# Performance work log

Measured on AMD Instinct MI355X. Metric: run time of the kernel, lower is better.

Reference implementation:

```python
import jax, jax.numpy as jnp
import numpy as np

LORA_DIM = 16          # hard-coded in module
LORA_TOKEN_INDEX = 1   # lora_dim*layer_sequence + 1 with layer_sequence=0
B, S, D, H = 4, 2048, 1024, 4096  # num_hiddens = 4*num_input (forced by view())


def setup_inputs() -> dict:
    key = jax.random.key(0)
    ks = jax.random.split(key, 6)
    x = jax.random.normal(ks[0], (B, S, D), dtype=jnp.float32)
    W1 = jax.random.normal(ks[1], (H, D), dtype=jnp.float32) * 0.02
    b1 = jnp.zeros((H,), dtype=jnp.float32)
    W2 = jax.random.normal(ks[2], (D, H), dtype=jnp.float32) * 0.02
    b2 = jnp.zeros((D,), dtype=jnp.float32)
    scale = jnp.asarray(0.001, dtype=jnp.float32)  # nn.Parameter(torch.tensor(0.001))
    return {"x": x, "W1": W1, "b1": b1, "W2": W2, "b2": b2, "scale": scale}


def reference(x, W1, b1, W2, b2, scale):
    Bx, Sx, Dx = x.shape
    Hx = W1.shape[0]  # = 4*Dx
    # 16 lora tokens starting at LORA_TOKEN_INDEX
    lt = jax.lax.dynamic_slice_in_dim(x, LORA_TOKEN_INDEX, LORA_DIM, axis=1)
    even = lt[:, ::2, :]  # (B, 8, D)
    odd = lt[:, 1::2, :]  # (B, 8, D)
    # per-sample low-rank weight updates:
    # result_multiplication[b,k] = outer(even[b,k], odd[b,k]) (D,D)
    # matrix1 = first 4 blocks stacked -> (B, 4D, D); matrix2 = last 4 reshaped -> (B, D, 4D)
    m1 = (even[:, :4, :, None] * odd[:, :4, None, :]).reshape(Bx, Hx, Dx)
    m2 = (even[:, 4:, :, None] * odd[:, 4:, None, :]).reshape(Bx, Dx, Hx)
    # x @ (W1 + scale*m1)^T + b1, fused without repeating W1 per batch
    h = jnp.einsum('bsd,hd->bsh', x, W1) + scale * jnp.einsum('bsd,bhd->bsh', x, m1) + b1
    h = jax.nn.gelu(h, approximate=False)  # torch nn.GELU default = exact erf
    out = jnp.einsum('bsh,oh->bso', h, W2) + scale * jnp.einsum('bsh,boh->bso', h, m2) + b2
    return out
```

## Files before the change

kernel.cpp:

```cpp
#include <hip/hip_runtime.h>
#include <cstdint>
#include <cstddef>

#define MROWS 8192
#define DDIM  1024
#define HDIM  4096

typedef __bf16 bf16x8 __attribute__((ext_vector_type(8)));
typedef float  f32x4  __attribute__((ext_vector_type(4)));

typedef __attribute__((address_space(1))) void* as1_vp;
typedef __attribute__((address_space(3))) void* as3_vp;

__device__ __forceinline__ unsigned short f2bf(float f) {
  unsigned int u = __builtin_bit_cast(unsigned int, f);
  u += 0x7fffu + ((u >> 16) & 1u);
  return (unsigned short)(u >> 16);
}
__device__ __forceinline__ float bf2f(unsigned short h) {
  return __builtin_bit_cast(float, (unsigned int)h << 16);
}

__device__ __forceinline__ float fast_gelu(float x) {
  float x3 = x * x * x;
  float z = 0.7978845608028654f * x + 0.03567740814f * x3;
  float e = __builtin_amdgcn_exp2f(z * 2.8853900817779268f);
  float t = 1.0f - 2.0f * __builtin_amdgcn_rcpf(e + 1.0f);
  return 0.5f * x * (1.0f + t);
}

__device__ __forceinline__ void gld_lds16(const unsigned short* g, unsigned short* lds) {
  __builtin_amdgcn_global_load_lds((as1_vp)(uintptr_t)g, (as3_vp)lds, 16, 0, 0);
}

#define VMW(n) asm volatile("s_waitcnt vmcnt(" #n ")" ::: "memory")
#define LKW()  asm volatile("s_waitcnt lgkmcnt(0)" ::: "memory")
#define BAR()  asm volatile("s_barrier" ::: "memory")

__global__ __launch_bounds__(256) void pre_kernel(
    const float* __restrict__ x, const float* __restrict__ w1,
    const float* __restrict__ w2, unsigned short* __restrict__ xb,
    unsigned short* __restrict__ w1b, unsigned short* __restrict__ w2b,
    float* __restrict__ p1) {
  if (blockIdx.x < 8192) {
    int i = blockIdx.x * 256 + threadIdx.x;
    const float* src; unsigned short* dst; int off;
    if (i < 1048576) { src = w1; dst = w1b; off = i; }
    else             { src = w2; dst = w2b; off = i - 1048576; }
    float4 v = ((const float4*)src)[off];
    ushort4 o;
    o.x = f2bf(v.x); o.y = f2bf(v.y); o.z = f2bf(v.z); o.w = f2bf(v.w);
    ((ushort4*)dst)[off] = o;
    return;
  }
  const int bid = blockIdx.x - 8192;
  const int wave = threadIdx.x >> 6, lane = threadIdx.x & 63;
  const int m = bid * 4 + wave;
  const int b = m >> 11;
  const float4* xrow4 = (const float4*)(x + (size_t)m * DDIM);
  const float4* od4   = (const float4*)(x + ((size_t)b * 2048 + 2) * DDIM);
  ushort4* xbrow4 = (ushort4*)(xb + (size_t)m * DDIM);
  float a0 = 0.f, a1 = 0.f, a2 = 0.f, a3 = 0.f;
#pragma unroll
  for (int it = 0; it < 4; ++it) {
    int g = it * 64 + lane;
    float4 v = xrow4[g];
    ushort4 o; o.x = f2bf(v.x); o.y = f2bf(v.y); o.z = f2bf(v.z); o.w = f2bf(v.w);
    xbrow4[g] = o;
    float4 o0 = od4[g];
    float4 o1 = od4[512 + g];
    float4 o2 = od4[1024 + g];
    float4 o3 = od4[1536 + g];
    a0 += v.x * o0.x + v.y * o0.y + v.z * o0.z + v.w * o0.w;
    a1 += v.x * o1.x + v.y * o1.y + v.z * o1.z + v.w * o1.w;
    a2 += v.x * o2.x + v.y * o2.y + v.z * o2.z + v.w * o2.w;
    a3 += v.x * o3.x + v.y * o3.y + v.z * o3.z + v.w * o3.w;
  }
#pragma unroll
  for (int off = 32; off > 0; off >>= 1) {
    a0 += __shfl_down(a0, off);
    a1 += __shfl_down(a1, off);
    a2 += __shfl_down(a2, off);
    a3 += __shfl_down(a3, off);
  }
  if (lane == 0) {
    float4 r; r.x = a0; r.y = a1; r.z = a2; r.w = a3;
    ((float4*)p1)[m] = r;
  }
}

__global__ __launch_bounds__(512, 2) void gemm1_kernel(
    const unsigned short* __restrict__ xb, const unsigned short* __restrict__ w1b,
    const float* __restrict__ x, const float* __restrict__ b1,
    const float* __restrict__ p1, const float* __restrict__ scale_p,
    unsigned short* __restrict__ hact) {
  __shared__ __align__(16) unsigned short As[4 * 256 * 32];
  __shared__ __align__(16) unsigned short Bs[4 * 256 * 32];

  const int id = blockIdx.x;
  const int xcd = id & 7, w = id >> 3;
  const int m0 = (xcd * 4 + (w & 3)) * 256;
  const int n0 = (w >> 2) * 256;

  const int tid  = threadIdx.x;
  const int wave = tid >> 6, lane = tid & 63;
  const int quad = lane >> 4, l16 = lane & 15;
  const int wm2  = wave >> 2;
  const int wn2  = wave & 3;

  const unsigned short *gA0, *gA1, *gB0, *gB1;
  {
    int idx = tid;
    int r = idx >> 2, sl = idx & 3, c = (sl - (r >> 1)) & 3;
    gA0 = xb  + (size_t)(m0 + r) * DDIM + c * 8;
    gB0 = w1b + (size_t)(n0 + r) * DDIM + c * 8;
    idx = 512 + tid;
    r = idx >> 2; sl = idx & 3; c = (sl - (r >> 1)) & 3;
    gA1 = xb  + (size_t)(m0 + r) * DDIM + c * 8;
    gB1 = w1b + (size_t)(n0 + r) * DDIM + c * 8;
  }
  const int ldsOff0 = (wave * 64) * 8;
  const int ldsOff1 = (512 + wave * 64) * 8;

#define STAGE1(tt, sb) do {                                   \
    const int _k = (tt) * 32;                                 \
    unsigned short* _a = &As[(sb) * 8192];                    \
    unsigned short* _b = &Bs[(sb) * 8192];                    \
    gld_lds16(gA0 + _k, _a + ldsOff0);                        \
    gld_lds16(gA1 + _k, _a + ldsOff1);                        \
    gld_lds16(gB0 + _k, _b + ldsOff0);                        \
    gld_lds16(gB1 + _k, _b + ldsOff1);                        \
  } while (0)

  f32x4 acc[8][4];
  const f32x4 z = {0.f, 0.f, 0.f, 0.f};
#pragma unroll
  for (int i = 0; i < 8; ++i)
#pragma unroll
    for (int j = 0; j < 4; ++j) acc[i][j] = z;

  auto compute_tile = [&](const unsigned short* __restrict__ Ab,
                          const unsigned short* __restrict__ Bb) {
    bf16x8 a[8], b[4];
#pragma unroll
    for (int j = 0; j < 4; ++j) {
      const int rb = wn2 * 64 + j * 16 + l16;
      b[j] = *(const bf16x8*)(Bb + rb * 32 + ((quad + (rb >> 1)) & 3) * 8);
    }
#pragma unroll
    for (int i = 0; i < 8; ++i) {
      const int ra = wm2 * 128 + i * 16 + l16;
      a[i] = *(const bf16x8*)(Ab + ra * 32 + ((quad + (ra >> 1)) & 3) * 8);
    }
    __builtin_amdgcn_s_setprio(1);
#pragma unroll
    for (int i = 0; i < 8; ++i)
#pragma unroll
      for (int j = 0; j < 4; ++j)
        acc[i][j] = __builtin_amdgcn_mfma_f32_16x16x32_bf16(a[i], b[j], acc[i][j], 0, 0, 0);
    __builtin_amdgcn_s_setprio(0);
  };

#define TILE_FULL(tt, cb, sb) do {                            \
    STAGE1((tt) + 3, sb);                                     \
    VMW(12);                                                  \
    BAR();                                                    \
    compute_tile(&As[(cb) * 8192], &Bs[(cb) * 8192]);         \
    LKW();                                                    \
    BAR();                                                    \
  } while (0)

  STAGE1(0, 0);
  STAGE1(1, 1);
  STAGE1(2, 2);

#pragma unroll 1
  for (int t = 0; t < 28; t += 4) {
    TILE_FULL(t + 0, 0, 3);
    TILE_FULL(t + 1, 1, 0);
    TILE_FULL(t + 2, 2, 1);
    TILE_FULL(t + 3, 3, 2);
  }
  TILE_FULL(28, 0, 3);
  VMW(8);  BAR(); compute_tile(&As[1 * 8192], &Bs[1 * 8192]);
  VMW(4);  BAR(); compute_tile(&As[2 * 8192], &Bs[2 * 8192]);
  VMW(0);  BAR(); compute_tile(&As[3 * 8192], &Bs[3 * 8192]);

  const float sc = scale_p[0];
  const int bidx = m0 >> 11;
  const int i1 = (n0 + wn2 * 64) >> 10;
  const float* exrow = x + ((size_t)(bidx * 2048 + 1 + 2 * i1)) * DDIM;

  float exv[4], b1v[4]; int nn[4];
#pragma unroll
  for (int j = 0; j < 4; ++j) {
    nn[j]  = n0 + wn2 * 64 + j * 16 + l16;
    exv[j] = exrow[nn[j] & 1023];
    b1v[j] = b1[nn[j]];
  }
#pragma unroll
  for (int i = 0; i < 8; ++i) {
#pragma unroll
    for (int r = 0; r < 4; ++r) {
      const int m = m0 + wm2 * 128 + i * 16 + quad * 4 + r;
      const float pv = p1[(size_t)m * 4 + i1] * sc;
#pragma unroll
      for (int j = 0; j < 4; ++j) {
        float v = acc[i][j][r] + b1v[j] + pv * exv[j];
        hact[(size_t)m * HDIM + nn[j]] = f2bf(fast_gelu(v));
      }
    }
  }
#undef TILE_FULL
#undef STAGE1
}

__global__ __launch_bounds__(512, 2) void gemm2_kernel(
    const unsigned short* __restrict__ hact, const unsigned short* __restrict__ w2b,
    const float* __restrict__ x, const float* __restrict__ b2,
    const float* __restrict__ scale_p, float* __restrict__ out) {
  __shared__ __align__(16) unsigned short As[3 * 256 * 64];
  __shared__ __align__(16) unsigned short Bs[3 * 128 * 64];
  __shared__ __align__(16) unsigned short od_lds[1024];
  __shared__ __align__(16) float p2s[256 * 4];

  const int id = blockIdx.x;
  const int xcd = id & 7, w = id >> 3;
  const int m0 = (xcd * 4 + (w & 3)) * 256;
  const int n0 = (w >> 2) * 128;
  const int tid = threadIdx.x;
  const int wave = tid >> 6, lane = tid & 63, quad = lane >> 4, l16 = lane & 15;
  const int wmq = (wave >> 1) * 64;
  const int wnq = (wave & 1) * 64;
  const bool hi = (wave & 1);
  const int bidx = m0 >> 11;
  const int i2 = n0 >> 8;

  if (tid < 256) {
    const float4* src = (const float4*)(x + ((size_t)(bidx * 2048 + 10 + 2 * i2)) * DDIM);
    float4 v = src[tid];
    ushort4 o; o.x = f2bf(v.x); o.y = f2bf(v.y); o.z = f2bf(v.z); o.w = f2bf(v.w);
    ((ushort4*)od_lds)[tid] = o;
  }
  LKW();

  f32x4 acc[4][4];
  const f32x4 z = {0.f, 0.f, 0.f, 0.f};
#pragma unroll
  for (int i = 0; i < 4; ++i)
#pragma unroll
    for (int j = 0; j < 4; ++j) acc[i][j] = z;
  f32x4 pacc[2] = {z, z};
  const bf16x8 zer8 = __builtin_bit_cast(bf16x8, z);

  const unsigned short *gA[4], *gB[2];
#pragma unroll
  for (int s = 0; s < 4; ++s) {
    int idx = (wave * 4 + s) * 64 + lane;
    int r = idx >> 3, sl = idx & 7, c = (sl - r) & 7;
    gA[s] = hact + (size_t)(m0 + r) * HDIM + c * 8;
  }
#pragma unroll
  for (int s = 0; s < 2; ++s) {
    int idx = (wave * 2 + s) * 64 + lane;
    int r = idx >> 3, sl = idx & 7, c = (sl - r) & 7;
    gB[s] = w2b + (size_t)(n0 + r) * HDIM + c * 8;
  }

#define STAGE2(tt, sb) do {                                   \
    const int _k = (tt) * 64;                                 \
    unsigned short* _a = &As[(sb) * 16384];                   \
    unsigned short* _b = &Bs[(sb) * 8192];                    \
    gld_lds16(gA[0] + _k, _a + (wave * 4 + 0) * 512);         \
    gld_lds16(gA[1] + _k, _a + (wave * 4 + 1) * 512);         \
    gld_lds16(gA[2] + _k, _a + (wave * 4 + 2) * 512);         \
    gld_lds16(gA[3] + _k, _a + (wave * 4 + 3) * 512);         \
    gld_lds16(gB[0] + _k, _b + (wave * 2 + 0) * 512);         \
    gld_lds16(gB[1] + _k, _b + (wave * 2 + 1) * 512);         \
  } while (0)

  auto compute_tile = [&](const unsigned short* __restrict__ Ab,
                          const unsigned short* __restrict__ Bb, int odk) {
#pragma unroll
    for (int kk = 0; kk < 64; kk += 32) {
      bf16x8 a[4], b[4];
      const int cb = (kk >> 3) + quad;
#pragma unroll
      for (int j = 0; j < 4; ++j) {
        const int rb = wnq + j * 16 + l16;
        b[j] = *(const bf16x8*)(Bb + rb * 64 + ((cb + rb) & 7) * 8);
      }
#pragma unroll
      for (int i = 0; i < 4; ++i) {
        const int ra = wmq + i * 16 + l16;
        a[i] = *(const bf16x8*)(Ab + ra * 64 + ((cb + ra) & 7) * 8);
      }
      {
        bf16x8 odv = *(const bf16x8*)(od_lds + odk + kk + quad * 8);
        bf16x8 bod = (l16 == 0) ? odv : zer8;
        bf16x8 pa0 = hi ? a[2] : a[0];
        bf16x8 pa1 = hi ? a[3] : a[1];
        pacc[0] = __builtin_amdgcn_mfma_f32_16x16x32_bf16(pa0, bod, pacc[0], 0, 0, 0);
        pacc[1] = __builtin_amdgcn_mfma_f32_16x16x32_bf16(pa1, bod, pacc[1], 0, 0, 0);
      }
      __builtin_amdgcn_s_setprio(1);
#pragma unroll
      for (int i = 0; i < 4; ++i)
#pragma unroll
        for (int j = 0; j < 4; ++j)
          acc[i][j] = __builtin_amdgcn_mfma_f32_16x16x32_bf16(a[i], b[j], acc[i][j], 0, 0, 0);
      __builtin_amdgcn_s_setprio(0);
    }
  };

  auto flush_p2 = [&](int seg) {
    const int ibase = hi ? 2 : 0;
    if (l16 == 0) {
#pragma unroll
      for (int ip = 0; ip < 2; ++ip)
#pragma unroll
        for (int e = 0; e < 4; ++e)
          p2s[(wmq + (ibase + ip) * 16 + quad * 4 + e) * 4 + seg] = pacc[ip][e];
    }
    pacc[0] = z; pacc[1] = z;
  };

#define TF2(tt, cb, sb) do {                                  \
    STAGE2((tt) + 2, sb);                                     \
    VMW(12);                                                  \
    BAR();                                                    \
    compute_tile(&As[(cb) * 16384], &Bs[(cb) * 8192], ((tt) * 64) & 1023); \
    if (((tt) & 15) == 15) flush_p2((tt) >> 4);               \
    LKW();                                                    \
    BAR();                                                    \
  } while (0)

  STAGE2(0, 0);
  STAGE2(1, 1);

#pragma unroll 1
  for (int t = 0; t < 60; t += 3) {
    TF2(t + 0, 0, 2);
    TF2(t + 1, 1, 0);
    TF2(t + 2, 2, 1);
  }
  TF2(60, 0, 2);
  TF2(61, 1, 0);
  VMW(6);  BAR(); compute_tile(&As[2 * 16384], &Bs[2 * 8192], 896);
  VMW(0);  BAR(); compute_tile(&As[0 * 16384], &Bs[0 * 8192], 960);
  flush_p2(3);
  LKW();
  BAR();

  const float sc = scale_p[0];
  const float* evrow = x + ((size_t)(bidx * 2048 + 9 + 2 * i2)) * DDIM;

  float4 ev[4]; float b2v[4]; int nn[4];
#pragma unroll
  for (int j = 0; j < 4; ++j) {
    nn[j] = n0 + wnq + j * 16 + l16;
    ev[j]  = *(const float4*)(evrow + 4 * (nn[j] & 255));
    b2v[j] = b2[nn[j]];
  }
#pragma unroll
  for (int i = 0; i < 4; ++i) {
#pragma unroll
    for (int r = 0; r < 4; ++r) {
      const int mloc = wmq + i * 16 + quad * 4 + r;
      const int m = m0 + mloc;
      const float4 pv = *(const float4*)(p2s + mloc * 4);
#pragma unroll
      for (int j = 0; j < 4; ++j) {
        float lora = ev[j].x * pv.x + ev[j].y * pv.y + ev[j].z * pv.z + ev[j].w * pv.w;
        out[(size_t)m * DDIM + nn[j]] = acc[i][j][r] + b2v[j] + sc * lora;
      }
    }
  }
#undef TF2
#undef STAGE2
}

extern "C" void kernel_launch(void* const* d_in, const int* in_sizes, int n_in,
                              void* d_out, int out_size, void* d_ws, size_t ws_size,
                              hipStream_t stream) {
  const float* x     = (const float*)d_in[0];
  const float* W1    = (const float*)d_in[1];
  const float* b1    = (const float*)d_in[2];
  const float* W2    = (const float*)d_in[3];
  const float* b2    = (const float*)d_in[4];
  const float* scale = (const float*)d_in[5];
  float* out = (float*)d_out;

  char* ws = (char*)d_ws;
  unsigned short* xb   = (unsigned short*)(ws);
  unsigned short* w1b  = (unsigned short*)(ws + 16777216);
  unsigned short* w2b  = (unsigned short*)(ws + 25165824);
  unsigned short* hact = (unsigned short*)(ws + 33554432);
  float*          p1   = (float*)(ws + 100663296);

  pre_kernel<<<dim3(10240), dim3(256), 0, stream>>>(x, W1, W2, xb, w1b, w2b, p1);
  gemm1_kernel<<<dim3(512), dim3(512), 0, stream>>>(xb, w1b, x, b1, p1, scale, hact);
  gemm2_kernel<<<dim3(256), dim3(512), 0, stream>>>(hact, w2b, x, b2, scale, out);
}
```

Baseline: 280.7 us.

## Software-pipeline LDS fragment reads against MFMA in both GEMM main loops

```diff
diff --git a/kernel.cpp b/kernel.cpp
--- a/kernel.cpp
+++ b/kernel.cpp
@@ -139,52 +139,76 @@
 #pragma unroll
     for (int j = 0; j < 4; ++j) acc[i][j] = z;
 
-  auto compute_tile = [&](const unsigned short* __restrict__ Ab,
-                          const unsigned short* __restrict__ Bb) {
-    bf16x8 a[8], b[4];
+  bf16x8 a[8], b[4];
+
+  auto RA = [&](int nb) {
+    const unsigned short* Ab = As + nb * 8192;
+    const unsigned short* Bb = Bs + nb * 8192;
 #pragma unroll
     for (int j = 0; j < 4; ++j) {
       const int rb = wn2 * 64 + j * 16 + l16;
       b[j] = *(const bf16x8*)(Bb + rb * 32 + ((quad + (rb >> 1)) & 3) * 8);
     }
 #pragma unroll
-    for (int i = 0; i < 8; ++i) {
+    for (int i = 0; i < 4; ++i) {
       const int ra = wm2 * 128 + i * 16 + l16;
       a[i] = *(const bf16x8*)(Ab + ra * 32 + ((quad + (ra >> 1)) & 3) * 8);
     }
+  };
+  auto RB = [&](int cb) {
+    const unsigned short* Ab = As + cb * 8192;
+#pragma unroll
+    for (int i = 4; i < 8; ++i) {
+      const int ra = wm2 * 128 + i * 16 + l16;
+      a[i] = *(const bf16x8*)(Ab + ra * 32 + ((quad + (ra >> 1)) & 3) * 8);
+    }
+  };
+  auto MFA = [&]() {
     __builtin_amdgcn_s_setprio(1);
 #pragma unroll
-    for (int i = 0; i < 8; ++i)
+    for (int i = 0; i < 4; ++i)
 #pragma unroll
       for (int j = 0; j < 4; ++j)
         acc[i][j] = __builtin_amdgcn_mfma_f32_16x16x32_bf16(a[i], b[j], acc[i][j], 0, 0, 0);
     __builtin_amdgcn_s_setprio(0);
   };
-
-#define TILE_FULL(tt, cb, sb) do {                            \
-    STAGE1((tt) + 3, sb);                                     \
-    VMW(12);                                                  \
-    BAR();                                                    \
-    compute_tile(&As[(cb) * 8192], &Bs[(cb) * 8192]);         \
-    LKW();                                                    \
-    BAR();                                                    \
+  auto MFB = [&]() {
+    __builtin_amdgcn_s_setprio(1);
+#pragma unroll
+    for (int i = 4; i < 8; ++i)
+#pragma unroll
+      for (int j = 0; j < 4; ++j)
+        acc[i][j] = __builtin_amdgcn_mfma_f32_16x16x32_bf16(a[i], b[j], acc[i][j], 0, 0, 0);
+    __builtin_amdgcn_s_setprio(0);
+  };
+
+#define G1BODY(cb, sb, nb, tt) do {   \
+    LKW(); MFA();                     \
+    RB(cb);                           \
+    STAGE1((tt) + 3, sb);             \
+    VMW(8);                           \
+    LKW(); MFB();                     \
+    BAR();                            \
+    RA(nb);                           \
   } while (0)
 
   STAGE1(0, 0);
   STAGE1(1, 1);
   STAGE1(2, 2);
+  VMW(8); BAR();
+  RA(0);
 
 #pragma unroll 1
   for (int t = 0; t < 28; t += 4) {
-    TILE_FULL(t + 0, 0, 3);
-    TILE_FULL(t + 1, 1, 0);
-    TILE_FULL(t + 2, 2, 1);
-    TILE_FULL(t + 3, 3, 2);
-  }
-  TILE_FULL(28, 0, 3);
-  VMW(8);  BAR(); compute_tile(&As[1 * 8192], &Bs[1 * 8192]);
-  VMW(4);  BAR(); compute_tile(&As[2 * 8192], &Bs[2 * 8192]);
-  VMW(0);  BAR(); compute_tile(&As[3 * 8192], &Bs[3 * 8192]);
+    G1BODY(0, 3, 1, t + 0);
+    G1BODY(1, 0, 2, t + 1);
+    G1BODY(2, 1, 3, t + 2);
+    G1BODY(3, 2, 0, t + 3);
+  }
+  LKW(); MFA(); RB(0); STAGE1(31, 3); VMW(8); LKW(); MFB(); BAR(); RA(1);
+  LKW(); MFA(); RB(1); VMW(4); LKW(); MFB(); BAR(); RA(2);
+  LKW(); MFA(); RB(2); VMW(0); LKW(); MFB(); BAR(); RA(3);
+  LKW(); MFA(); RB(3); LKW(); MFB();
 
   const float sc = scale_p[0];
   const int bidx = m0 >> 11;
@@ -211,7 +235,7 @@
       }
     }
   }
-#undef TILE_FULL
+#undef G1BODY
 #undef STAGE1
 }
 
@@ -279,40 +303,38 @@
     gld_lds16(gB[1] + _k, _b + (wave * 2 + 1) * 512);         \
   } while (0)
 
-  auto compute_tile = [&](const unsigned short* __restrict__ Ab,
-                          const unsigned short* __restrict__ Bb, int odk) {
-#pragma unroll
-    for (int kk = 0; kk < 64; kk += 32) {
-      bf16x8 a[4], b[4];
-      const int cb = (kk >> 3) + quad;
-#pragma unroll
-      for (int j = 0; j < 4; ++j) {
-        const int rb = wnq + j * 16 + l16;
-        b[j] = *(const bf16x8*)(Bb + rb * 64 + ((cb + rb) & 7) * 8);
-      }
-#pragma unroll
-      for (int i = 0; i < 4; ++i) {
-        const int ra = wmq + i * 16 + l16;
-        a[i] = *(const bf16x8*)(Ab + ra * 64 + ((cb + ra) & 7) * 8);
-      }
-      {
-        bf16x8 odv = *(const bf16x8*)(od_lds + odk + kk + quad * 8);
-        bf16x8 bod = (l16 == 0) ? odv : zer8;
-        bf16x8 pa0 = hi ? a[2] : a[0];
-        bf16x8 pa1 = hi ? a[3] : a[1];
-        pacc[0] = __builtin_amdgcn_mfma_f32_16x16x32_bf16(pa0, bod, pacc[0], 0, 0, 0);
-        pacc[1] = __builtin_amdgcn_mfma_f32_16x16x32_bf16(pa1, bod, pacc[1], 0, 0, 0);
-      }
-      __builtin_amdgcn_s_setprio(1);
-#pragma unroll
-      for (int i = 0; i < 4; ++i)
-#pragma unroll
-        for (int j = 0; j < 4; ++j)
-          acc[i][j] = __builtin_amdgcn_mfma_f32_16x16x32_bf16(a[i], b[j], acc[i][j], 0, 0, 0);
-      __builtin_amdgcn_s_setprio(0);
-    }
-  };
-
+  bf16x8 a[4], b[4], odv;
+
+  auto RPH = [&](int nb, int kk, int odk) {
+    const unsigned short* Ab = As + nb * 16384;
+    const unsigned short* Bb = Bs + nb * 8192;
+    odv = *(const bf16x8*)(od_lds + odk + kk + quad * 8);
+    const int cb = (kk >> 3) + quad;
+#pragma unroll
+    for (int j = 0; j < 4; ++j) {
+      const int rb = wnq + j * 16 + l16;
+      b[j] = *(const bf16x8*)(Bb + rb * 64 + ((cb + rb) & 7) * 8);
+    }
+#pragma unroll
+    for (int i = 0; i < 4; ++i) {
+      const int ra = wmq + i * 16 + l16;
+      a[i] = *(const bf16x8*)(Ab + ra * 64 + ((cb + ra) & 7) * 8);
+    }
+  };
+  auto MPH = [&]() {
+    bf16x8 bod = (l16 == 0) ? odv : zer8;
+    bf16x8 pa0 = hi ? a[2] : a[0];
+    bf16x8 pa1 = hi ? a[3] : a[1];
+    pacc[0] = __builtin_amdgcn_mfma_f32_16x16x32_bf16(pa0, bod, pacc[0], 0, 0, 0);
+    pacc[1] = __builtin_amdgcn_mfma_f32_16x16x32_bf16(pa1, bod, pacc[1], 0, 0, 0);
+    __builtin_amdgcn_s_setprio(1);
+#pragma unroll
+    for (int i = 0; i < 4; ++i)
+#pragma unroll
+      for (int j = 0; j < 4; ++j)
+        acc[i][j] = __builtin_amdgcn_mfma_f32_16x16x32_bf16(a[i], b[j], acc[i][j], 0, 0, 0);
+    __builtin_amdgcn_s_setprio(0);
+  };
   auto flush_p2 = [&](int seg) {
     const int ibase = hi ? 2 : 0;
     if (l16 == 0) {
@@ -325,29 +347,36 @@
     pacc[0] = z; pacc[1] = z;
   };
 
-#define TF2(tt, cb, sb) do {                                  \
-    STAGE2((tt) + 2, sb);                                     \
-    VMW(12);                                                  \
-    BAR();                                                    \
-    compute_tile(&As[(cb) * 16384], &Bs[(cb) * 8192], ((tt) * 64) & 1023); \
-    if (((tt) & 15) == 15) flush_p2((tt) >> 4);               \
-    LKW();                                                    \
-    BAR();                                                    \
+#define G2BODY(cb, sb, nb, tt) do {                 \
+    LKW(); MPH();                                   \
+    RPH(cb, 32, ((tt) * 64) & 1023);                \
+    STAGE2((tt) + 2, sb);                           \
+    VMW(6);                                         \
+    LKW(); MPH();                                   \
+    if (((tt) & 15) == 15) flush_p2((tt) >> 4);     \
+    BAR();                                          \
+    RPH(nb, 0, (((tt) + 1) * 64) & 1023);           \
   } while (0)
 
   STAGE2(0, 0);
   STAGE2(1, 1);
+  VMW(6); BAR();
+  RPH(0, 0, 0);
 
 #pragma unroll 1
   for (int t = 0; t < 60; t += 3) {
-    TF2(t + 0, 0, 2);
-    TF2(t + 1, 1, 0);
-    TF2(t + 2, 2, 1);
-  }
-  TF2(60, 0, 2);
-  TF2(61, 1, 0);
-  VMW(6);  BAR(); compute_tile(&As[2 * 16384], &Bs[2 * 8192], 896);
-  VMW(0);  BAR(); compute_tile(&As[0 * 16384], &Bs[0 * 8192], 960);
+    G2BODY(0, 2, 1, t + 0);
+    G2BODY(1, 0, 2, t + 1);
+    G2BODY(2, 1, 0, t + 2);
+  }
+  LKW(); MPH(); RPH(0, 32, (60 * 64) & 1023); STAGE2(62, 2); VMW(6);
+  LKW(); MPH(); BAR(); RPH(1, 0, (61 * 64) & 1023);
+  LKW(); MPH(); RPH(1, 32, (61 * 64) & 1023); STAGE2(63, 0); VMW(6);
+  LKW(); MPH(); BAR(); RPH(2, 0, (62 * 64) & 1023);
+  LKW(); MPH(); RPH(2, 32, (62 * 64) & 1023); VMW(0);
+  LKW(); MPH(); BAR(); RPH(0, 0, (63 * 64) & 1023);
+  LKW(); MPH(); RPH(0, 32, (63 * 64) & 1023);
+  LKW(); MPH();
   flush_p2(3);
   LKW();
   BAR();
@@ -376,7 +405,7 @@
       }
     }
   }
-#undef TF2
+#undef G2BODY
 #undef STAGE2
 }
 
```

After: 255.9 us. -8.8%, faster.

## Restructure gemm1 main loop into 8-phase ping-pong schedule with interleaved staging

Applied to the files above, without the earlier changes.

```diff
diff --git a/kernel.cpp b/kernel.cpp
--- a/kernel.cpp
+++ b/kernel.cpp
@@ -16,9 +16,6 @@
   unsigned int u = __builtin_bit_cast(unsigned int, f);
   u += 0x7fffu + ((u >> 16) & 1u);
   return (unsigned short)(u >> 16);
-}
-__device__ __forceinline__ float bf2f(unsigned short h) {
-  return __builtin_bit_cast(float, (unsigned int)h << 16);
 }
 
 __device__ __forceinline__ float fast_gelu(float x) {
@@ -33,9 +30,9 @@
   __builtin_amdgcn_global_load_lds((as1_vp)(uintptr_t)g, (as3_vp)lds, 16, 0, 0);
 }
 
-#define VMW(n) asm volatile("s_waitcnt vmcnt(" #n ")" ::: "memory")
-#define LKW()  asm volatile("s_waitcnt lgkmcnt(0)" ::: "memory")
-#define BAR()  asm volatile("s_barrier" ::: "memory")
+#define VMW(n)  asm volatile("s_waitcnt vmcnt(" #n ")" ::: "memory")
+#define LKW()   asm volatile("s_waitcnt lgkmcnt(0)" ::: "memory")
+#define BAR()   asm volatile("s_barrier" ::: "memory")
 
 __global__ __launch_bounds__(256) void pre_kernel(
     const float* __restrict__ x, const float* __restrict__ w1,
@@ -94,8 +91,8 @@
     const float* __restrict__ x, const float* __restrict__ b1,
     const float* __restrict__ p1, const float* __restrict__ scale_p,
     unsigned short* __restrict__ hact) {
-  __shared__ __align__(16) unsigned short As[4 * 256 * 32];
-  __shared__ __align__(16) unsigned short Bs[4 * 256 * 32];
+  __shared__ __align__(16) unsigned short As[4 * 8192];
+  __shared__ __align__(16) unsigned short Bs[4 * 8192];
 
   const int id = blockIdx.x;
   const int xcd = id & 7, w = id >> 3;
@@ -122,14 +119,17 @@
   const int ldsOff0 = (wave * 64) * 8;
   const int ldsOff1 = (512 + wave * 64) * 8;
 
-#define STAGE1(tt, sb) do {                                   \
-    const int _k = (tt) * 32;                                 \
-    unsigned short* _a = &As[(sb) * 8192];                    \
-    unsigned short* _b = &Bs[(sb) * 8192];                    \
-    gld_lds16(gA0 + _k, _a + ldsOff0);                        \
-    gld_lds16(gA1 + _k, _a + ldsOff1);                        \
-    gld_lds16(gB0 + _k, _b + ldsOff0);                        \
-    gld_lds16(gB1 + _k, _b + ldsOff1);                        \
+#define STG_A(tt, hh, bb) do {                                      \
+    const int _o = (tt) * 64 + (hh) * 32;                           \
+    unsigned short* _d = As + ((bb) * 2 + (hh)) * 8192;             \
+    gld_lds16(gA0 + _o, _d + ldsOff0);                              \
+    gld_lds16(gA1 + _o, _d + ldsOff1);                              \
+  } while (0)
+#define STG_B(tt, hh, bb) do {                                      \
+    const int _o = (tt) * 64 + (hh) * 32;                           \
+    unsigned short* _d = Bs + ((bb) * 2 + (hh)) * 8192;             \
+    gld_lds16(gB0 + _o, _d + ldsOff0);                              \
+    gld_lds16(gB1 + _o, _d + ldsOff1);                              \
   } while (0)
 
   f32x4 acc[8][4];
@@ -139,52 +139,95 @@
 #pragma unroll
     for (int j = 0; j < 4; ++j) acc[i][j] = z;
 
-  auto compute_tile = [&](const unsigned short* __restrict__ Ab,
-                          const unsigned short* __restrict__ Bb) {
-    bf16x8 a[8], b[4];
+  bf16x8 aS0[4], aS1[4], bS0[4], bS1[4];
+
+  auto LDB4 = [&](const unsigned short* Bh, bf16x8 (&bb)[4]) {
 #pragma unroll
     for (int j = 0; j < 4; ++j) {
       const int rb = wn2 * 64 + j * 16 + l16;
-      b[j] = *(const bf16x8*)(Bb + rb * 32 + ((quad + (rb >> 1)) & 3) * 8);
-    }
-#pragma unroll
-    for (int i = 0; i < 8; ++i) {
-      const int ra = wm2 * 128 + i * 16 + l16;
-      a[i] = *(const bf16x8*)(Ab + ra * 32 + ((quad + (ra >> 1)) & 3) * 8);
-    }
+      bb[j] = *(const bf16x8*)(Bh + rb * 32 + ((quad + (rb >> 1)) & 3) * 8);
+    }
+  };
+  auto LDA4 = [&](const unsigned short* Ah, int i0, bf16x8 (&aa)[4]) {
+#pragma unroll
+    for (int i = 0; i < 4; ++i) {
+      const int ra = wm2 * 128 + (i0 + i) * 16 + l16;
+      aa[i] = *(const bf16x8*)(Ah + ra * 32 + ((quad + (ra >> 1)) & 3) * 8);
+    }
+  };
+  auto MF16 = [&](int i0, bf16x8 (&aa)[4], bf16x8 (&bb)[4]) {
     __builtin_amdgcn_s_setprio(1);
 #pragma unroll
-    for (int i = 0; i < 8; ++i)
+    for (int i = 0; i < 4; ++i)
 #pragma unroll
       for (int j = 0; j < 4; ++j)
-        acc[i][j] = __builtin_amdgcn_mfma_f32_16x16x32_bf16(a[i], b[j], acc[i][j], 0, 0, 0);
+        acc[i0 + i][j] = __builtin_amdgcn_mfma_f32_16x16x32_bf16(aa[i], bb[j], acc[i0 + i][j], 0, 0, 0);
     __builtin_amdgcn_s_setprio(0);
   };
 
-#define TILE_FULL(tt, cb, sb) do {                            \
-    STAGE1((tt) + 3, sb);                                     \
-    VMW(12);                                                  \
-    BAR();                                                    \
-    compute_tile(&As[(cb) * 8192], &Bs[(cb) * 8192]);         \
-    LKW();                                                    \
-    BAR();                                                    \
-  } while (0)
-
-  STAGE1(0, 0);
-  STAGE1(1, 1);
-  STAGE1(2, 2);
+  const unsigned short* A0lo = As;
+  const unsigned short* A0hi = As + 8192;
+  const unsigned short* A1lo = As + 16384;
+  const unsigned short* A1hi = As + 24576;
+  const unsigned short* B0lo = Bs;
+  const unsigned short* B0hi = Bs + 8192;
+  const unsigned short* B1lo = Bs + 16384;
+  const unsigned short* B1hi = Bs + 24576;
+
+  STG_B(0, 0, 0); STG_A(0, 0, 0); STG_B(0, 1, 0); STG_A(0, 1, 0);
+  STG_B(1, 0, 1); STG_A(1, 0, 1); STG_B(1, 1, 1);
+  VMW(6); BAR();
 
 #pragma unroll 1
-  for (int t = 0; t < 28; t += 4) {
-    TILE_FULL(t + 0, 0, 3);
-    TILE_FULL(t + 1, 1, 0);
-    TILE_FULL(t + 2, 2, 1);
-    TILE_FULL(t + 3, 3, 2);
-  }
-  TILE_FULL(28, 0, 3);
-  VMW(8);  BAR(); compute_tile(&As[1 * 8192], &Bs[1 * 8192]);
-  VMW(4);  BAR(); compute_tile(&As[2 * 8192], &Bs[2 * 8192]);
-  VMW(0);  BAR(); compute_tile(&As[3 * 8192], &Bs[3 * 8192]);
+  for (int it = 0; it < 7; ++it) {
+    const int T = 2 * it;
+    LDB4(B0lo, bS0); LDA4(A0lo, 0, aS0);
+    STG_A(T + 1, 1, 1);
+    BAR(); LKW(); MF16(0, aS0, bS0); BAR();
+    LDA4(A0lo, 4, aS1);
+    STG_B(T + 2, 0, 0);
+    BAR(); LKW(); MF16(4, aS1, bS0); BAR();
+    LDB4(B0hi, bS1); LDA4(A0hi, 0, aS0);
+    STG_A(T + 2, 0, 0);
+    BAR(); LKW(); MF16(0, aS0, bS1); BAR();
+    LDA4(A0hi, 4, aS1);
+    STG_B(T + 2, 1, 0);
+    VMW(6);
+    BAR(); LKW(); MF16(4, aS1, bS1); BAR();
+    LDB4(B1lo, bS0); LDA4(A1lo, 0, aS0);
+    STG_A(T + 2, 1, 0);
+    BAR(); LKW(); MF16(0, aS0, bS0); BAR();
+    LDA4(A1lo, 4, aS1);
+    STG_B(T + 3, 0, 1);
+    BAR(); LKW(); MF16(4, aS1, bS0); BAR();
+    LDB4(B1hi, bS1); LDA4(A1hi, 0, aS0);
+    STG_A(T + 3, 0, 1);
+    BAR(); LKW(); MF16(0, aS0, bS1); BAR();
+    LDA4(A1hi, 4, aS1);
+    STG_B(T + 3, 1, 1);
+    VMW(6);
+    BAR(); LKW(); MF16(4, aS1, bS1); BAR();
+  }
+  {
+    LDB4(B0lo, bS0); LDA4(A0lo, 0, aS0);
+    STG_A(15, 1, 1);
+    BAR(); LKW(); MF16(0, aS0, bS0); BAR();
+    LDA4(A0lo, 4, aS1);
+    BAR(); LKW(); MF16(4, aS1, bS0); BAR();
+    LDB4(B0hi, bS1); LDA4(A0hi, 0, aS0);
+    BAR(); LKW(); MF16(0, aS0, bS1); BAR();
+    LDA4(A0hi, 4, aS1);
+    VMW(0);
+    BAR(); LKW(); MF16(4, aS1, bS1); BAR();
+    LDB4(B1lo, bS0); LDA4(A1lo, 0, aS0);
+    BAR(); LKW(); MF16(0, aS0, bS0); BAR();
+    LDA4(A1lo, 4, aS1);
+    BAR(); LKW(); MF16(4, aS1, bS0); BAR();
+    LDB4(B1hi, bS1); LDA4(A1hi, 0, aS0);
+    BAR(); LKW(); MF16(0, aS0, bS1); BAR();
+    LDA4(A1hi, 4, aS1);
+    LKW(); MF16(4, aS1, bS1);
+  }
 
   const float sc = scale_p[0];
   const int bidx = m0 >> 11;
@@ -211,8 +254,8 @@
       }
     }
   }
-#undef TILE_FULL
-#undef STAGE1
+#undef STG_A
+#undef STG_B
 }
 
 __global__ __launch_bounds__(512, 2) void gemm2_kernel(
@@ -327,7 +370,7 @@
 
 #define TF2(tt, cb, sb) do {                                  \
     STAGE2((tt) + 2, sb);                                     \
-    VMW(12);                                                  \
+    VMW(6);                                                   \
     BAR();                                                    \
     compute_tile(&As[(cb) * 16384], &Bs[(cb) * 8192], ((tt) * 64) & 1023); \
     if (((tt) & 15) == 15) flush_p2((tt) >> 4);               \
@@ -347,6 +390,7 @@
   TF2(60, 0, 2);
   TF2(61, 1, 0);
   VMW(6);  BAR(); compute_tile(&As[2 * 16384], &Bs[2 * 8192], 896);
+  LKW();   BAR();
   VMW(0);  BAR(); compute_tile(&As[0 * 16384], &Bs[0 * 8192], 960);
   flush_p2(3);
   LKW();
```

Measured after the change: 281.0 us. Within noise of the previous version (+0.1%).
